# Performance work log

Measured on AMD Instinct MI355X. Metric: run time of the kernel, lower is better.

The kernel has to match this reference:

```python
import jax, jax.numpy as jnp
import numpy as np

H = 64
VOCAB = 128
LN_EPS = 1e-5
NORM_EPS = 1e-12


def _l2norm(k):
    # F.normalize(..., dim=-1): x / max(||x||_2, eps)
    n = jnp.sqrt(jnp.sum(k * k, axis=-1, keepdims=True))
    return k / jnp.maximum(n, NORM_EPS)


def _delta_scan(M0, ks, vs):
    # ks, vs: [L, B, H] time-major; M0: [B, H, H]
    def step(M, kv):
        k, v = kv
        Mk = jnp.einsum('bij,bj->bi', M, k)            # [B,H]
        M = M + (v - Mk)[:, :, None] * k[:, None, :]   # rank-1 update
        return M, None
    M, _ = jax.lax.scan(step, M0, (ks, vs))
    return M


def reference(x, embed, W1, b1, W2, b2, ln_g, ln_b, Wk, Wv, Wq, Wattn, Wout, bout):
    # Encoder: embed -> residual FF -> LayerNorm
    h = embed[x]                                        # [B,L,H]
    ff = jnp.maximum(h @ W1.T + b1, 0.0) @ W2.T + b2
    z = h + ff
    mu = jnp.mean(z, axis=-1, keepdims=True)
    var = jnp.mean((z - mu) ** 2, axis=-1, keepdims=True)
    hidden = (z - mu) / jnp.sqrt(var + LN_EPS) * ln_g + ln_b  # [B,L,H]

    B, L, _ = hidden.shape
    # First delta-rule memory write over all L steps
    ks = _l2norm(hidden @ Wk.T)                         # [B,L,H]
    vs = hidden @ Wv.T                                  # [B,L,H]
    M0 = jnp.zeros((B, H, H), dtype=hidden.dtype)
    M = _delta_scan(M0, jnp.swapaxes(ks, 0, 1), jnp.swapaxes(vs, 0, 1))

    half = L // 2
    slots = jnp.swapaxes(M, 1, 2)                       # [B,H,H] = M^T
    q = hidden[:, :half, :] @ Wattn.T                   # [B,half,H]
    # bmm(q, slots^T) = q @ M
    attn = jax.nn.softmax(jnp.einsum('bth,bhk->btk', q, M) / jnp.sqrt(jnp.asarray(H, hidden.dtype)), axis=-1)
    ctx = jnp.einsum('btk,bkh->bth', attn, slots)       # [B,half,H]

    # Second delta-rule write seeded from M
    ks2 = _l2norm(ctx @ Wk.T)
    vs2 = ctx @ Wv.T
    M2 = _delta_scan(M, jnp.swapaxes(ks2, 0, 1), jnp.swapaxes(vs2, 0, 1))

    q_last = hidden[:, -1, :] @ Wq.T                    # [B,H]
    read = jnp.einsum('bij,bj->bi', M2, q_last)         # [B,H]
    return read @ Wout.T + bout                         # [B,VOCAB]


def setup_inputs() -> dict:
    key = jax.random.key(0)
    ks = jax.random.split(key, 16)
    B, L = 64, 4096
    s = 0.05
    return {
        'x': jax.random.randint(ks[0], (B, L), 0, VOCAB),
        'embed': jax.random.normal(ks[1], (VOCAB, H), jnp.float32) * s,
        'W1': jax.random.normal(ks[2], (2 * H, H), jnp.float32) * s,
        'b1': jnp.zeros((2 * H,), jnp.float32),
        'W2': jax.random.normal(ks[3], (H, 2 * H), jnp.float32) * s,
        'b2': jnp.zeros((H,), jnp.float32),
        'ln_g': jnp.ones((H,), jnp.float32),
        'ln_b': jnp.zeros((H,), jnp.float32),
        'Wk': jax.random.normal(ks[4], (H, H), jnp.float32) * s,
        'Wv': jax.random.normal(ks[5], (H, H), jnp.float32) * s,
        'Wq': jax.random.normal(ks[6], (H, H), jnp.float32) * s,
        'Wattn': jax.random.normal(ks[7], (H, H), jnp.float32) * s,
        'Wout': jax.random.normal(ks[8], (VOCAB, H), jnp.float32) * s,
        'bout': jnp.zeros((VOCAB,), jnp.float32),
    }
```

## Files before the change

### kernel.cpp

```cpp
#include <hip/hip_runtime.h>

#define SEQL 4096
#define NB 64

__device__ __forceinline__ float dpp_xor1_add(float x) {
    int v = __builtin_amdgcn_mov_dpp(__float_as_int(x), 0xB1, 0xF, 0xF, true);
    return x + __int_as_float(v);
}
__device__ __forceinline__ float dpp_xor2_add(float x) {
    int v = __builtin_amdgcn_mov_dpp(__float_as_int(x), 0x4E, 0xF, 0xF, true);
    return x + __int_as_float(v);
}

#define FMA16(A, W, H)                                      \
    A[0]  = fmaf(W.x, H.x, A[0]);  A[1]  = fmaf(W.x, H.y, A[1]);   \
    A[2]  = fmaf(W.x, H.z, A[2]);  A[3]  = fmaf(W.x, H.w, A[3]);   \
    A[4]  = fmaf(W.y, H.x, A[4]);  A[5]  = fmaf(W.y, H.y, A[5]);   \
    A[6]  = fmaf(W.y, H.z, A[6]);  A[7]  = fmaf(W.y, H.w, A[7]);   \
    A[8]  = fmaf(W.z, H.x, A[8]);  A[9]  = fmaf(W.z, H.y, A[9]);   \
    A[10] = fmaf(W.z, H.z, A[10]); A[11] = fmaf(W.z, H.w, A[11]);  \
    A[12] = fmaf(W.w, H.x, A[12]); A[13] = fmaf(W.w, H.y, A[13]);  \
    A[14] = fmaf(W.w, H.z, A[14]); A[15] = fmaf(W.w, H.w, A[15])

__device__ __forceinline__ void proj_tile64(const float* __restrict__ sW,
                                            const float* __restrict__ sA,
                                            int jq, int tq, float* __restrict__ a)
{
#pragma unroll
    for (int u = 0; u < 16; ++u) a[u] = 0.f;
#pragma unroll 4
    for (int i = 0; i < 64; ++i) {
        float4 w  = *reinterpret_cast<const float4*>(&sW[i * 68 + jq]);
        float4 h4 = *reinterpret_cast<const float4*>(&sA[i * 68 + tq]);
        FMA16(a, w, h4);
    }
}

__device__ __forceinline__ void load_w_t(const float* __restrict__ W, int ldw, int col0,
                                         int tid, float4* __restrict__ r)
{
    const int j = tid & 63;
    const int cq0 = tid >> 6;
#pragma unroll
    for (int it = 0; it < 4; ++it)
        r[it] = *reinterpret_cast<const float4*>(&W[(size_t)j * ldw + col0 + (it * 4 + cq0) * 4]);
}
__device__ __forceinline__ void write_w_t(const float4* __restrict__ r,
                                          float* __restrict__ sWb, int tid)
{
    const int j = tid & 63;
    const int cq0 = tid >> 6;
#pragma unroll
    for (int it = 0; it < 4; ++it) {
        const int c = (it * 4 + cq0) * 4;
        sWb[(c + 0) * 68 + j] = r[it].x;
        sWb[(c + 1) * 68 + j] = r[it].y;
        sWb[(c + 2) * 68 + j] = r[it].z;
        sWb[(c + 3) * 68 + j] = r[it].w;
    }
}

__device__ __forceinline__ void stage_w_t(const float* __restrict__ W, int ldw, int col0,
                                          float* __restrict__ sWb, int tid)
{
    float4 r[4];
    load_w_t(W, ldw, col0, tid, r);
    write_w_t(r, sWb, tid);
}
__device__ __forceinline__ void stage_w_n(const float* __restrict__ W,
                                          float* __restrict__ sWb, int tid)
{
#pragma unroll
    for (int it = 0; it < 4; ++it) {
        int item = it * 256 + tid;
        int r = item >> 4, c4 = item & 15;
        float4 w = *reinterpret_cast<const float4*>(&W[(size_t)r * 64 + c4 * 4]);
        *reinterpret_cast<float4*>(&sWb[r * 68 + c4 * 4]) = w;
    }
}

__global__ __launch_bounds__(256) void encoder_kernel(
    const int* __restrict__ x, const float* __restrict__ embed,
    const float* __restrict__ W1, const float* __restrict__ b1,
    const float* __restrict__ W2, const float* __restrict__ b2,
    const float* __restrict__ ln_g, const float* __restrict__ ln_b,
    const float* __restrict__ Wk, const float* __restrict__ Wv,
    const float* __restrict__ Wq,
    float* __restrict__ ks, float* __restrict__ vs,
    float* __restrict__ hidT, float* __restrict__ qlast)
{
    __shared__ __align__(16) float sZ[64 * 68];
    __shared__ __align__(16) float sF[64 * 68];
    __shared__ __align__(16) float sW[64 * 68];

    const int tid = threadIdx.x;
    const size_t g0 = (size_t)blockIdx.x * 64;
    const int b = (int)(g0 >> 12);
    const int l0 = (int)(g0 & (SEQL - 1));
    const int jq = (tid & 15) * 4;
    const int tq = (tid >> 4) * 4;
    const bool doq = (l0 < 2048);
    const bool dolast = (l0 == SEQL - 64);

    float4 pf[4], pf2[4];

    load_w_t(W1, 64, 0, tid, pf);
    for (int idx = tid; idx < 4096; idx += 256) {
        int t = idx >> 6, i = idx & 63;
        sZ[i * 68 + t] = embed[(size_t)x[g0 + t] * 64 + i];
    }
    write_w_t(pf, sW, tid);
    load_w_t(W2, 128, 0, tid, pf2);
    __syncthreads();

    float zacc[16];
#pragma unroll
    for (int u = 0; u < 16; ++u) zacc[u] = 0.f;

    {
        float a[16];
        proj_tile64(sW, sZ, jq, tq, a);
        float4 bb = *reinterpret_cast<const float4*>(&b1[jq]);
        float bv[4] = {bb.x, bb.y, bb.z, bb.w};
#pragma unroll
        for (int u = 0; u < 4; ++u) {
            float4 o;
            o.x = fmaxf(a[u * 4 + 0] + bv[u], 0.f);
            o.y = fmaxf(a[u * 4 + 1] + bv[u], 0.f);
            o.z = fmaxf(a[u * 4 + 2] + bv[u], 0.f);
            o.w = fmaxf(a[u * 4 + 3] + bv[u], 0.f);
            *reinterpret_cast<float4*>(&sF[(jq + u) * 68 + tq]) = o;
        }
    }
    __syncthreads();
    write_w_t(pf2, sW, tid);
    load_w_t(W1 + 4096, 64, 0, tid, pf);
    __syncthreads();
#pragma unroll 4
    for (int p = 0; p < 64; ++p) {
        float4 w  = *reinterpret_cast<const float4*>(&sW[p * 68 + jq]);
        float4 f4 = *reinterpret_cast<const float4*>(&sF[p * 68 + tq]);
        FMA16(zacc, w, f4);
    }
    __syncthreads();
    write_w_t(pf, sW, tid);
    load_w_t(W2, 128, 64, tid, pf2);
    __syncthreads();
    {
        float a[16];
        proj_tile64(sW, sZ, jq, tq, a);
        float4 bb = *reinterpret_cast<const float4*>(&b1[64 + jq]);
        float bv[4] = {bb.x, bb.y, bb.z, bb.w};
#pragma unroll
        for (int u = 0; u < 4; ++u) {
            float4 o;
            o.x = fmaxf(a[u * 4 + 0] + bv[u], 0.f);
            o.y = fmaxf(a[u * 4 + 1] + bv[u], 0.f);
            o.z = fmaxf(a[u * 4 + 2] + bv[u], 0.f);
            o.w = fmaxf(a[u * 4 + 3] + bv[u], 0.f);
            *reinterpret_cast<float4*>(&sF[(jq + u) * 68 + tq]) = o;
        }
    }
    __syncthreads();
    write_w_t(pf2, sW, tid);
    load_w_t(Wk, 64, 0, tid, pf);
    load_w_t(Wv, 64, 0, tid, pf2);
    __syncthreads();
#pragma unroll 4
    for (int p = 0; p < 64; ++p) {
        float4 w  = *reinterpret_cast<const float4*>(&sW[p * 68 + jq]);
        float4 f4 = *reinterpret_cast<const float4*>(&sF[p * 68 + tq]);
        FMA16(zacc, w, f4);
    }

    {
        float z[16];
        float4 b2v = *reinterpret_cast<const float4*>(&b2[jq]);
        float bv[4] = {b2v.x, b2v.y, b2v.z, b2v.w};
#pragma unroll
        for (int u = 0; u < 4; ++u) {
            float4 h4 = *reinterpret_cast<const float4*>(&sZ[(jq + u) * 68 + tq]);
            z[u * 4 + 0] = h4.x + bv[u] + zacc[u * 4 + 0];
            z[u * 4 + 1] = h4.y + bv[u] + zacc[u * 4 + 1];
            z[u * 4 + 2] = h4.z + bv[u] + zacc[u * 4 + 2];
            z[u * 4 + 3] = h4.w + bv[u] + zacc[u * 4 + 3];
        }
        float s[4], ss[4];
#pragma unroll
        for (int v = 0; v < 4; ++v) {
            s[v]  = z[v] + z[4 + v] + z[8 + v] + z[12 + v];
            ss[v] = z[v] * z[v] + z[4 + v] * z[4 + v]
                  + z[8 + v] * z[8 + v] + z[12 + v] * z[12 + v];
        }
#pragma unroll
        for (int m = 1; m <= 8; m <<= 1) {
#pragma unroll
            for (int v = 0; v < 4; ++v) {
                s[v]  += __shfl_xor(s[v], m);
                ss[v] += __shfl_xor(ss[v], m);
            }
        }
        float mu[4], inv[4];
#pragma unroll
        for (int v = 0; v < 4; ++v) {
            mu[v] = s[v] * 0.015625f;
            float var = ss[v] * 0.015625f - mu[v] * mu[v];
            inv[v] = rsqrtf(var + 1e-5f);
        }
        float4 g4  = *reinterpret_cast<const float4*>(&ln_g[jq]);
        float4 be4 = *reinterpret_cast<const float4*>(&ln_b[jq]);
        float gv[4] = {g4.x, g4.y, g4.z, g4.w};
        float bev[4] = {be4.x, be4.y, be4.z, be4.w};
#pragma unroll
        for (int u = 0; u < 4; ++u) {
            float4 o;
            o.x = (z[u * 4 + 0] - mu[0]) * inv[0] * gv[u] + bev[u];
            o.y = (z[u * 4 + 1] - mu[1]) * inv[1] * gv[u] + bev[u];
            o.z = (z[u * 4 + 2] - mu[2]) * inv[2] * gv[u] + bev[u];
            o.w = (z[u * 4 + 3] - mu[3]) * inv[3] * gv[u] + bev[u];
            *reinterpret_cast<float4*>(&sZ[(jq + u) * 68 + tq]) = o;
        }
    }
    __syncthreads();
    write_w_t(pf, sW, tid);
    write_w_t(pf2, sF, tid);
    if (dolast) load_w_t(Wq, 64, 0, tid, pf);
    __syncthreads();

    {
        float a[16];
        proj_tile64(sW, sZ, jq, tq, a);
        float ssq[4];
#pragma unroll
        for (int v = 0; v < 4; ++v)
            ssq[v] = a[v] * a[v] + a[4 + v] * a[4 + v]
                   + a[8 + v] * a[8 + v] + a[12 + v] * a[12 + v];
#pragma unroll
        for (int m = 1; m <= 8; m <<= 1) {
#pragma unroll
            for (int v = 0; v < 4; ++v) ssq[v] += __shfl_xor(ssq[v], m);
        }
#pragma unroll
        for (int v = 0; v < 4; ++v) {
            float sc = 1.f / fmaxf(sqrtf(ssq[v]), 1e-12f);
            float4 o = make_float4(a[v] * sc, a[4 + v] * sc, a[8 + v] * sc, a[12 + v] * sc);
            *reinterpret_cast<float4*>(&ks[(g0 + tq + v) * 64 + jq]) = o;
        }
    }
    {
        float a[16];
        proj_tile64(sF, sZ, jq, tq, a);
#pragma unroll
        for (int v = 0; v < 4; ++v) {
            float4 o = make_float4(a[v], a[4 + v], a[8 + v], a[12 + v]);
            *reinterpret_cast<float4*>(&vs[(g0 + tq + v) * 64 + jq]) = o;
        }
    }

    if (doq) {
#pragma unroll
        for (int it = 0; it < 4; ++it) {
            int item = it * 256 + tid;
            int i = item >> 4, q4 = (item & 15) * 4;
            float4 v = *reinterpret_cast<const float4*>(&sZ[i * 68 + q4]);
            *reinterpret_cast<float4*>(&hidT[((size_t)b * 64 + i) * 2048 + l0 + q4]) = v;
        }
    }

    if (dolast) {
        __syncthreads();
        write_w_t(pf, sW, tid);
        __syncthreads();
        float a[16];
        proj_tile64(sW, sZ, jq, tq, a);
        if ((tid >> 4) == 15) {
            float4 o = make_float4(a[3], a[7], a[11], a[15]);
            *reinterpret_cast<float4*>(&qlast[(size_t)b * 64 + jq]) = o;
        }
    }
}

__global__ __launch_bounds__(256) void precompute_kernel(
    const float* __restrict__ Mbuf, const float* __restrict__ Wattn,
    const float* __restrict__ Wk, const float* __restrict__ Wv,
    float* __restrict__ WAM, float* __restrict__ MK, float* __restrict__ MV)
{
    __shared__ __align__(16) float sM[64 * 68];
    __shared__ __align__(16) float sOp[64 * 68];
    const int b = blockIdx.x;
    const int tid = threadIdx.x;
    const int jq = (tid & 15) * 4;
    const int tq = (tid >> 4) * 4;
    const float* Mb = Mbuf + (size_t)b * 4096;

    stage_w_n(Mb, sM, tid);
    stage_w_n(Wattn, sOp, tid);
    __syncthreads();
    {
        float a[16];
        proj_tile64(sM, sOp, jq, tq, a);
#pragma unroll
        for (int v = 0; v < 4; ++v)
            *reinterpret_cast<float4*>(&WAM[(size_t)b * 4096 + (tq + v) * 64 + jq]) =
                make_float4(a[v], a[4 + v], a[8 + v], a[12 + v]);
    }
    __syncthreads();
    stage_w_t(Wk, 64, 0, sOp, tid);
    __syncthreads();
    {
        float a[16];
        proj_tile64(sM, sOp, jq, tq, a);
#pragma unroll
        for (int v = 0; v < 4; ++v)
            *reinterpret_cast<float4*>(&MK[(size_t)b * 4096 + (tq + v) * 64 + jq]) =
                make_float4(a[v], a[4 + v], a[8 + v], a[12 + v]);
    }
    __syncthreads();
    stage_w_t(Wv, 64, 0, sOp, tid);
    __syncthreads();
    {
        float a[16];
        proj_tile64(sM, sOp, jq, tq, a);
#pragma unroll
        for (int v = 0; v < 4; ++v)
            *reinterpret_cast<float4*>(&MV[(size_t)b * 4096 + (tq + v) * 64 + jq]) =
                make_float4(a[v], a[4 + v], a[8 + v], a[12 + v]);
    }
}

#define STEP2(K0, K1, K2, K3, V)                                                \
    do {                                                                        \
        float dp0 = fmaf(p[0], K0.x, fmaf(p[1], K0.y, fmaf(p[2], K0.z, p[3] * K0.w))); \
        float dp1 = fmaf(p[4], K1.x, fmaf(p[5], K1.y, fmaf(p[6], K1.z, p[7] * K1.w))); \
        float dp2 = fmaf(p[8], K2.x, fmaf(p[9], K2.y, fmaf(p[10], K2.z, p[11] * K2.w))); \
        float dp3 = fmaf(p[12], K3.x, fmaf(p[13], K3.y, fmaf(p[14], K3.z, p[15] * K3.w))); \
        float dq0 = fmaf(q[0], K0.x, fmaf(q[1], K0.y, fmaf(q[2], K0.z, q[3] * K0.w))); \
        float dq1 = fmaf(q[4], K1.x, fmaf(q[5], K1.y, fmaf(q[6], K1.z, q[7] * K1.w))); \
        float dq2 = fmaf(q[8], K2.x, fmaf(q[9], K2.y, fmaf(q[10], K2.z, q[11] * K2.w))); \
        float dq3 = fmaf(q[12], K3.x, fmaf(q[13], K3.y, fmaf(q[14], K3.z, q[15] * K3.w))); \
        float ddp = (dp0 + dp1) + (dp2 + dp3);                                  \
        float ddq = (dq0 + dq1) + (dq2 + dq3);                                  \
        ddp = dpp_xor1_add(ddp);  ddq = dpp_xor1_add(ddq);                      \
        ddp = dpp_xor2_add(ddp);  ddq = dpp_xor2_add(ddq);                      \
        float up = -ddp;                                                        \
        float uq = V - ddq;                                                     \
        p[0] = fmaf(up, K0.x, p[0]);   q[0] = fmaf(uq, K0.x, q[0]);             \
        p[1] = fmaf(up, K0.y, p[1]);   q[1] = fmaf(uq, K0.y, q[1]);             \
        p[2] = fmaf(up, K0.z, p[2]);   q[2] = fmaf(uq, K0.z, q[2]);             \
        p[3] = fmaf(up, K0.w, p[3]);   q[3] = fmaf(uq, K0.w, q[3]);             \
        p[4] = fmaf(up, K1.x, p[4]);   q[4] = fmaf(uq, K1.x, q[4]);             \
        p[5] = fmaf(up, K1.y, p[5]);   q[5] = fmaf(uq, K1.y, q[5]);             \
        p[6] = fmaf(up, K1.z, p[6]);   q[6] = fmaf(uq, K1.z, q[6]);             \
        p[7] = fmaf(up, K1.w, p[7]);   q[7] = fmaf(uq, K1.w, q[7]);             \
        p[8] = fmaf(up, K2.x, p[8]);   q[8] = fmaf(uq, K2.x, q[8]);             \
        p[9] = fmaf(up, K2.y, p[9]);   q[9] = fmaf(uq, K2.y, q[9]);             \
        p[10] = fmaf(up, K2.z, p[10]); q[10] = fmaf(uq, K2.z, q[10]);           \
        p[11] = fmaf(up, K2.w, p[11]); q[11] = fmaf(uq, K2.w, q[11]);           \
        p[12] = fmaf(up, K3.x, p[12]); q[12] = fmaf(uq, K3.x, q[12]);           \
        p[13] = fmaf(up, K3.y, p[13]); q[13] = fmaf(uq, K3.y, q[13]);           \
        p[14] = fmaf(up, K3.z, p[14]); q[14] = fmaf(uq, K3.z, q[14]);           \
        p[15] = fmaf(up, K3.w, p[15]); q[15] = fmaf(uq, K3.w, q[15]);           \
    } while (0)

__global__ __launch_bounds__(256) void chunk_kernel(
    float* __restrict__ ksb, float* __restrict__ vsb, int C)
{
    __shared__ __align__(16) float sk[2][32 * 64];
    __shared__ __align__(16) float sv[2][32 * 64];

    const int job = blockIdx.x;
    const int tid = threadIdx.x;
    const int r = tid >> 2;
    const int c0 = (tid & 3) * 16;
    float* kc = ksb + (size_t)job * C * 64;
    float* vc = vsb + (size_t)job * C * 64;

    float p[16], q[16];
#pragma unroll
    for (int j = 0; j < 16; ++j) { p[j] = (c0 + j == r) ? 1.f : 0.f; q[j] = 0.f; }

    const int nt = C >> 5;
    float4 rk0, rk1, rv0, rv1;

    {
        const float4* gk = reinterpret_cast<const float4*>(kc);
        const float4* gv = reinterpret_cast<const float4*>(vc);
        float4 a0 = gk[tid], a1 = gk[256 + tid];
        float4 b0 = gv[tid], b1 = gv[256 + tid];
        float4* dk = reinterpret_cast<float4*>(sk[0]);
        float4* dv = reinterpret_cast<float4*>(sv[0]);
        dk[tid] = a0; dk[256 + tid] = a1;
        dv[tid] = b0; dv[256 + tid] = b1;
    }
    if (nt > 1) {
        const float4* gk = reinterpret_cast<const float4*>(kc + 2048);
        const float4* gv = reinterpret_cast<const float4*>(vc + 2048);
        rk0 = gk[tid]; rk1 = gk[256 + tid];
        rv0 = gv[tid]; rv1 = gv[256 + tid];
    }
    __syncthreads();

    int cur = 0;
    for (int tile = 0; tile < nt; ++tile) {
        if (tile + 1 < nt) {
            float4* dk = reinterpret_cast<float4*>(sk[cur ^ 1]);
            float4* dv = reinterpret_cast<float4*>(sv[cur ^ 1]);
            dk[tid] = rk0; dk[256 + tid] = rk1;
            dv[tid] = rv0; dv[256 + tid] = rv1;
            if (tile + 2 < nt) {
                const float4* gk = reinterpret_cast<const float4*>(kc + (size_t)(tile + 2) * 2048);
                const float4* gv = reinterpret_cast<const float4*>(vc + (size_t)(tile + 2) * 2048);
                rk0 = gk[tid]; rk1 = gk[256 + tid];
                rv0 = gv[tid]; rv1 = gv[256 + tid];
            }
        }

        const float* kl = sk[cur] + c0;
        const float* vl = sv[cur] + r;
        float4 a0, a1, a2, a3, e0, e1, e2, e3;
        float va, ve;
        {
            const float4* kp = reinterpret_cast<const float4*>(kl);
            a0 = kp[0]; a1 = kp[1]; a2 = kp[2]; a3 = kp[3];
            va = vl[0];
        }
#pragma unroll
        for (int t = 0; t < 32; t += 2) {
            {
                const float4* kp = reinterpret_cast<const float4*>(kl + (t + 1) * 64);
                e0 = kp[0]; e1 = kp[1]; e2 = kp[2]; e3 = kp[3];
                ve = vl[(t + 1) * 64];
            }
            STEP2(a0, a1, a2, a3, va);
            if (t + 2 < 32) {
                const float4* kp = reinterpret_cast<const float4*>(kl + (t + 2) * 64);
                a0 = kp[0]; a1 = kp[1]; a2 = kp[2]; a3 = kp[3];
                va = vl[(t + 2) * 64];
            }
            STEP2(e0, e1, e2, e3, ve);
        }
        __syncthreads();
        cur ^= 1;
    }

    float4* po = reinterpret_cast<float4*>(kc + r * 64 + c0);
    po[0] = make_float4(p[0], p[1], p[2], p[3]);
    po[1] = make_float4(p[4], p[5], p[6], p[7]);
    po[2] = make_float4(p[8], p[9], p[10], p[11]);
    po[3] = make_float4(p[12], p[13], p[14], p[15]);
    float4* qo = reinterpret_cast<float4*>(vc + r * 64 + c0);
    qo[0] = make_float4(q[0], q[1], q[2], q[3]);
    qo[1] = make_float4(q[4], q[5], q[6], q[7]);
    qo[2] = make_float4(q[8], q[9], q[10], q[11]);
    qo[3] = make_float4(q[12], q[13], q[14], q[15]);
}

__global__ __launch_bounds__(256) void combine_kernel(
    const float* __restrict__ Pb, const float* __restrict__ Qb,
    const float* __restrict__ Min, float* __restrict__ Mout,
    int nc, int chunk_stride)
{
    __shared__ __align__(16) float sP[2][64 * 64];
    __shared__ __align__(16) float sM[2][16 * 68];
    const int bb = blockIdx.x;
    const int b = bb >> 2;
    const int r0 = (bb & 3) << 4;
    const int tid = threadIdx.x;
    const int rl = tid >> 4;
    const int j4 = (tid & 15) * 4;
    const int gr = r0 + rl;

    if (Min) {
        *reinterpret_cast<float4*>(&sM[0][rl * 68 + j4]) =
            *reinterpret_cast<const float4*>(Min + ((size_t)b * 64 + gr) * 64 + j4);
    } else {
        *reinterpret_cast<float4*>(&sM[0][rl * 68 + j4]) = make_float4(0.f, 0.f, 0.f, 0.f);
    }
    {
        const float4* g = reinterpret_cast<const float4*>(Pb + (size_t)b * nc * chunk_stride);
        float4* s = reinterpret_cast<float4*>(sP[0]);
        for (int i = tid; i < 1024; i += 256) s[i] = g[i];
    }
    __syncthreads();

    int cur = 0;
    for (int c = 0; c < nc; ++c) {
        const size_t cbase = (size_t)(b * nc + c) * chunk_stride;
        float4 rp0, rp1, rp2, rp3;
        if (c + 1 < nc) {
            const float4* g = reinterpret_cast<const float4*>(Pb + cbase + chunk_stride);
            rp0 = g[tid]; rp1 = g[tid + 256]; rp2 = g[tid + 512]; rp3 = g[tid + 768];
        }
        float4 rq = *reinterpret_cast<const float4*>(Qb + cbase + (size_t)gr * 64 + j4);

        float ax = 0.f, ay = 0.f, az = 0.f, aw = 0.f;
        const float* Mrow = &sM[cur][rl * 68];
        const float* Pl = sP[c & 1];
#pragma unroll 4
        for (int mg = 0; mg < 16; ++mg) {
            float4 a4 = *reinterpret_cast<const float4*>(Mrow + mg * 4);
            float4 p0 = *reinterpret_cast<const float4*>(Pl + (mg * 4 + 0) * 64 + j4);
            float4 p1 = *reinterpret_cast<const float4*>(Pl + (mg * 4 + 1) * 64 + j4);
            float4 p2 = *reinterpret_cast<const float4*>(Pl + (mg * 4 + 2) * 64 + j4);
            float4 p3 = *reinterpret_cast<const float4*>(Pl + (mg * 4 + 3) * 64 + j4);
            ax = fmaf(a4.x, p0.x, ax); ay = fmaf(a4.x, p0.y, ay);
            az = fmaf(a4.x, p0.z, az); aw = fmaf(a4.x, p0.w, aw);
            ax = fmaf(a4.y, p1.x, ax); ay = fmaf(a4.y, p1.y, ay);
            az = fmaf(a4.y, p1.z, az); aw = fmaf(a4.y, p1.w, aw);
            ax = fmaf(a4.z, p2.x, ax); ay = fmaf(a4.z, p2.y, ay);
            az = fmaf(a4.z, p2.z, az); aw = fmaf(a4.z, p2.w, aw);
            ax = fmaf(a4.w, p3.x, ax); ay = fmaf(a4.w, p3.y, ay);
            az = fmaf(a4.w, p3.z, az); aw = fmaf(a4.w, p3.w, aw);
        }
        const int nxt = cur ^ 1;
        *reinterpret_cast<float4*>(&sM[nxt][rl * 68 + j4]) =
            make_float4(ax + rq.x, ay + rq.y, az + rq.z, aw + rq.w);
        if (c + 1 < nc) {
            float4* s = reinterpret_cast<float4*>(sP[(c + 1) & 1]);
            s[tid] = rp0; s[tid + 256] = rp1; s[tid + 512] = rp2; s[tid + 768] = rp3;
        }
        __syncthreads();
        cur = nxt;
    }
    *reinterpret_cast<float4*>(Mout + ((size_t)b * 64 + gr) * 64 + j4) =
        *reinterpret_cast<const float4*>(&sM[cur][rl * 68 + j4]);
}

__global__ __launch_bounds__(256) void attn_kernel(
    const float* __restrict__ hidT, const float* __restrict__ WAM,
    const float* __restrict__ MK, const float* __restrict__ MV,
    float* __restrict__ ks2, float* __restrict__ vs2)
{
    __shared__ __align__(16) float sW1[64 * 68];
    __shared__ __align__(16) float sW2[64 * 68];
    __shared__ __align__(16) float sA[64 * 68];

    const int b = blockIdx.y;
    const int tile0 = blockIdx.x * 64;
    const int tid = threadIdx.x;
    const int jq = (tid & 15) * 4;
    const int tq = (tid >> 4) * 4;
    const size_t qbase = (size_t)b * 2048 + tile0;
    const float* hb = hidT + (size_t)b * 64 * 2048 + tile0;

    float4 pfk[4];
    stage_w_n(WAM + (size_t)b * 4096, sW1, tid);
    stage_w_t(MV + (size_t)b * 4096, 64, 0, sW2, tid);
#pragma unroll
    for (int it = 0; it < 4; ++it) {
        int item = it * 256 + tid;
        int i = item >> 4, q4 = (item & 15) * 4;
        float4 v = *reinterpret_cast<const float4*>(&hb[(size_t)i * 2048 + q4]);
        *reinterpret_cast<float4*>(&sA[i * 68 + q4]) = v;
    }
    load_w_t(MK + (size_t)b * 4096, 64, 0, tid, pfk);
    __syncthreads();

    float a[16];
    proj_tile64(sW1, sA, jq, tq, a);
#pragma unroll
    for (int u = 0; u < 16; ++u) a[u] *= 0.125f;

    {
        float mx[4], sm[4];
#pragma unroll
        for (int v = 0; v < 4; ++v)
            mx[v] = fmaxf(fmaxf(a[v], a[4 + v]), fmaxf(a[8 + v], a[12 + v]));
#pragma unroll
        for (int m = 1; m <= 8; m <<= 1) {
#pragma unroll
            for (int v = 0; v < 4; ++v) mx[v] = fmaxf(mx[v], __shfl_xor(mx[v], m));
        }
#pragma unroll
        for (int v = 0; v < 4; ++v) {
            a[v]      = __expf(a[v]      - mx[v]);
            a[4 + v]  = __expf(a[4 + v]  - mx[v]);
            a[8 + v]  = __expf(a[8 + v]  - mx[v]);
            a[12 + v] = __expf(a[12 + v] - mx[v]);
            sm[v] = a[v] + a[4 + v] + a[8 + v] + a[12 + v];
        }
#pragma unroll
        for (int m = 1; m <= 8; m <<= 1) {
#pragma unroll
            for (int v = 0; v < 4; ++v) sm[v] += __shfl_xor(sm[v], m);
        }
        float rinv[4];
#pragma unroll
        for (int v = 0; v < 4; ++v) rinv[v] = 1.f / sm[v];
#pragma unroll
        for (int v = 0; v < 4; ++v) {
            a[v] *= rinv[v]; a[4 + v] *= rinv[v];
            a[8 + v] *= rinv[v]; a[12 + v] *= rinv[v];
        }
    }
    __syncthreads();
#pragma unroll
    for (int u = 0; u < 4; ++u)
        *reinterpret_cast<float4*>(&sA[(jq + u) * 68 + tq]) =
            make_float4(a[u * 4 + 0], a[u * 4 + 1], a[u * 4 + 2], a[u * 4 + 3]);
    write_w_t(pfk, sW1, tid);
    __syncthreads();

    float ak[16], av[16];
#pragma unroll
    for (int u = 0; u < 16; ++u) { ak[u] = 0.f; av[u] = 0.f; }
#pragma unroll 2
    for (int i = 0; i < 64; ++i) {
        float4 wk = *reinterpret_cast<const float4*>(&sW1[i * 68 + jq]);
        float4 wv = *reinterpret_cast<const float4*>(&sW2[i * 68 + jq]);
        float4 p4 = *reinterpret_cast<const float4*>(&sA[i * 68 + tq]);
        FMA16(ak, wk, p4);
        FMA16(av, wv, p4);
    }

    {
        float ssq[4];
#pragma unroll
        for (int v = 0; v < 4; ++v)
            ssq[v] = ak[v] * ak[v] + ak[4 + v] * ak[4 + v]
                   + ak[8 + v] * ak[8 + v] + ak[12 + v] * ak[12 + v];
#pragma unroll
        for (int m = 1; m <= 8; m <<= 1) {
#pragma unroll
            for (int v = 0; v < 4; ++v) ssq[v] += __shfl_xor(ssq[v], m);
        }
#pragma unroll
        for (int v = 0; v < 4; ++v) {
            float sc = 1.f / fmaxf(sqrtf(ssq[v]), 1e-12f);
            const size_t o = (qbase + tq + v) * 64 + jq;
            *reinterpret_cast<float4*>(&ks2[o]) =
                make_float4(ak[v] * sc, ak[4 + v] * sc, ak[8 + v] * sc, ak[12 + v] * sc);
            *reinterpret_cast<float4*>(&vs2[o]) =
                make_float4(av[v], av[4 + v], av[8 + v], av[12 + v]);
        }
    }
}

__global__ __launch_bounds__(128) void out_kernel(
    const float* __restrict__ M2, const float* __restrict__ qlast,
    const float* __restrict__ Wout, const float* __restrict__ bout,
    float* __restrict__ out)
{
    const int b = blockIdx.x;
    const int tid = threadIdx.x;
    __shared__ float sq[64], sread[64];
    if (tid < 64) sq[tid] = qlast[b * 64 + tid];
    __syncthreads();
    if (tid < 64) {
        const float* Mr = M2 + ((size_t)b * 64 + tid) * 64;
        float acc = 0.f;
        for (int j = 0; j < 64; ++j) acc = fmaf(Mr[j], sq[j], acc);
        sread[tid] = acc;
    }
    __syncthreads();
    float acc = bout[tid];
    for (int h = 0; h < 64; ++h) acc = fmaf(Wout[tid * 64 + h], sread[h], acc);
    out[b * 128 + tid] = acc;
}

extern "C" void kernel_launch(void* const* d_in, const int* in_sizes, int n_in,
                              void* d_out, int out_size, void* d_ws, size_t ws_size,
                              hipStream_t stream)
{
    const int* x        = (const int*)d_in[0];
    const float* embed  = (const float*)d_in[1];
    const float* W1     = (const float*)d_in[2];
    const float* b1     = (const float*)d_in[3];
    const float* W2     = (const float*)d_in[4];
    const float* b2     = (const float*)d_in[5];
    const float* ln_g   = (const float*)d_in[6];
    const float* ln_b   = (const float*)d_in[7];
    const float* Wk     = (const float*)d_in[8];
    const float* Wv     = (const float*)d_in[9];
    const float* Wq     = (const float*)d_in[10];
    const float* Wattn  = (const float*)d_in[11];
    const float* Wout   = (const float*)d_in[12];
    const float* bout   = (const float*)d_in[13];

    float* ws = (float*)d_ws;
    float* ks  = ws;
    float* vs  = ks  + (size_t)NB * SEQL * 64;
    float* hid = vs  + (size_t)NB * SEQL * 64;
    float* ql  = hid + (size_t)NB * 2048 * 64;
    float* M   = ql  + (size_t)NB * 64;
    float* M2  = M   + (size_t)NB * 64 * 64;
    float* WAM = M2  + (size_t)NB * 64 * 64;
    float* MK  = WAM + (size_t)NB * 64 * 64;
    float* MV  = MK  + (size_t)NB * 64 * 64;
    if (ws_size < (size_t)(MV + (size_t)NB * 64 * 64 - ws) * sizeof(float)) return;

    hipLaunchKernelGGL(encoder_kernel, dim3((NB * SEQL) / 64), dim3(256), 0, stream,
                       x, embed, W1, b1, W2, b2, ln_g, ln_b, Wk, Wv, Wq,
                       ks, vs, hid, ql);

    const int C1 = 256, nc1 = SEQL / C1;
    hipLaunchKernelGGL(chunk_kernel, dim3(NB * nc1), dim3(256), 0, stream, ks, vs, C1);
    hipLaunchKernelGGL(combine_kernel, dim3(NB * 4), dim3(256), 0, stream,
                       ks, vs, (const float*)nullptr, M, nc1, C1 * 64);

    hipLaunchKernelGGL(precompute_kernel, dim3(NB), dim3(256), 0, stream,
                       M, Wattn, Wk, Wv, WAM, MK, MV);

    hipLaunchKernelGGL(attn_kernel, dim3(32, NB), dim3(256), 0, stream,
                       hid, WAM, MK, MV, ks, vs);

    const int C2 = 128, nc2 = 2048 / C2;
    hipLaunchKernelGGL(chunk_kernel, dim3(NB * nc2), dim3(256), 0, stream, ks, vs, C2);
    hipLaunchKernelGGL(combine_kernel, dim3(NB * 4), dim3(256), 0, stream,
                       ks, vs, M, M2, nc2, C2 * 64);

    hipLaunchKernelGGL(out_kernel, dim3(NB), dim3(128), 0, stream,
                       M2, ql, Wout, bout, (float*)d_out);
}
```

Baseline: 474.5 us.

## Fold second-scan combine into final readout via backward vector propagation

The second delta-rule pass no longer builds the full final memory matrix M2. The new final kernel starts from q_last and walks the chunk factors (P, Q) in reverse. Each step is a matrix-vector product, so the per-chunk matrix-matrix combine and its kernel launch are dropped. The second-pass chunk size also shrinks, giving more chunks and more parallel chunk work. The cost is a serial loop over more chunks, run by one block per batch, in the final kernel.

```diff
diff --git a/kernel.cpp b/kernel.cpp
--- a/kernel.cpp
+++ b/kernel.cpp
@@ -636,26 +636,87 @@
     }
 }
 
-__global__ __launch_bounds__(128) void out_kernel(
-    const float* __restrict__ M2, const float* __restrict__ qlast,
+__global__ __launch_bounds__(256) void final_kernel(
+    const float* __restrict__ Pb, const float* __restrict__ Qb,
+    const float* __restrict__ Mbuf, const float* __restrict__ qlast,
     const float* __restrict__ Wout, const float* __restrict__ bout,
-    float* __restrict__ out)
-{
+    float* __restrict__ out, int nc, int chunk_stride)
+{
+    __shared__ float s[64], qv[64], rv[64];
     const int b = blockIdx.x;
     const int tid = threadIdx.x;
-    __shared__ float sq[64], sread[64];
-    if (tid < 64) sq[tid] = qlast[b * 64 + tid];
-    __syncthreads();
-    if (tid < 64) {
-        const float* Mr = M2 + ((size_t)b * 64 + tid) * 64;
-        float acc = 0.f;
-        for (int j = 0; j < 64; ++j) acc = fmaf(Mr[j], sq[j], acc);
-        sread[tid] = acc;
-    }
-    __syncthreads();
-    float acc = bout[tid];
-    for (int h = 0; h < 64; ++h) acc = fmaf(Wout[tid * 64 + h], sread[h], acc);
-    out[b * 128 + tid] = acc;
+    const int r = tid >> 2;
+    const int c0 = (tid & 3) * 16;
+
+    if (tid < 64) { s[tid] = qlast[(size_t)b * 64 + tid]; qv[tid] = 0.f; }
+    __syncthreads();
+
+    for (int c = nc - 1; c >= 0; --c) {
+        const size_t base = (size_t)(b * nc + c) * chunk_stride + (size_t)r * 64 + c0;
+        const float4* gp = reinterpret_cast<const float4*>(Pb + base);
+        const float4* gq = reinterpret_cast<const float4*>(Qb + base);
+        float4 P0 = gp[0], P1 = gp[1], P2 = gp[2], P3 = gp[3];
+        float4 Q0 = gq[0], Q1 = gq[1], Q2 = gq[2], Q3 = gq[3];
+        const float4* sv4 = reinterpret_cast<const float4*>(&s[c0]);
+        float4 s0 = sv4[0], s1 = sv4[1], s2 = sv4[2], s3 = sv4[3];
+
+        float dp = 0.f, dq = 0.f;
+        dp = fmaf(P0.x, s0.x, dp); dp = fmaf(P0.y, s0.y, dp);
+        dp = fmaf(P0.z, s0.z, dp); dp = fmaf(P0.w, s0.w, dp);
+        dp = fmaf(P1.x, s1.x, dp); dp = fmaf(P1.y, s1.y, dp);
+        dp = fmaf(P1.z, s1.z, dp); dp = fmaf(P1.w, s1.w, dp);
+        dp = fmaf(P2.x, s2.x, dp); dp = fmaf(P2.y, s2.y, dp);
+        dp = fmaf(P2.z, s2.z, dp); dp = fmaf(P2.w, s2.w, dp);
+        dp = fmaf(P3.x, s3.x, dp); dp = fmaf(P3.y, s3.y, dp);
+        dp = fmaf(P3.z, s3.z, dp); dp = fmaf(P3.w, s3.w, dp);
+        dq = fmaf(Q0.x, s0.x, dq); dq = fmaf(Q0.y, s0.y, dq);
+        dq = fmaf(Q0.z, s0.z, dq); dq = fmaf(Q0.w, s0.w, dq);
+        dq = fmaf(Q1.x, s1.x, dq); dq = fmaf(Q1.y, s1.y, dq);
+        dq = fmaf(Q1.z, s1.z, dq); dq = fmaf(Q1.w, s1.w, dq);
+        dq = fmaf(Q2.x, s2.x, dq); dq = fmaf(Q2.y, s2.y, dq);
+        dq = fmaf(Q2.z, s2.z, dq); dq = fmaf(Q2.w, s2.w, dq);
+        dq = fmaf(Q3.x, s3.x, dq); dq = fmaf(Q3.y, s3.y, dq);
+        dq = fmaf(Q3.z, s3.z, dq); dq = fmaf(Q3.w, s3.w, dq);
+        dp = dpp_xor1_add(dp); dp = dpp_xor2_add(dp);
+        dq = dpp_xor1_add(dq); dq = dpp_xor2_add(dq);
+
+        __syncthreads();
+        if ((tid & 3) == 0) { s[r] = dp; qv[r] += dq; }
+        __syncthreads();
+    }
+
+    {
+        const float4* gm = reinterpret_cast<const float4*>(
+            Mbuf + (size_t)b * 4096 + (size_t)r * 64 + c0);
+        float4 M0 = gm[0], M1 = gm[1], M2v = gm[2], M3 = gm[3];
+        const float4* sv4 = reinterpret_cast<const float4*>(&s[c0]);
+        float4 s0 = sv4[0], s1 = sv4[1], s2 = sv4[2], s3 = sv4[3];
+        float d = 0.f;
+        d = fmaf(M0.x, s0.x, d); d = fmaf(M0.y, s0.y, d);
+        d = fmaf(M0.z, s0.z, d); d = fmaf(M0.w, s0.w, d);
+        d = fmaf(M1.x, s1.x, d); d = fmaf(M1.y, s1.y, d);
+        d = fmaf(M1.z, s1.z, d); d = fmaf(M1.w, s1.w, d);
+        d = fmaf(M2v.x, s2.x, d); d = fmaf(M2v.y, s2.y, d);
+        d = fmaf(M2v.z, s2.z, d); d = fmaf(M2v.w, s2.w, d);
+        d = fmaf(M3.x, s3.x, d); d = fmaf(M3.y, s3.y, d);
+        d = fmaf(M3.z, s3.z, d); d = fmaf(M3.w, s3.w, d);
+        d = dpp_xor1_add(d); d = dpp_xor2_add(d);
+        if ((tid & 3) == 0) rv[r] = d + qv[r];
+    }
+    __syncthreads();
+
+    if (tid < 128) {
+        const float* wr = Wout + (size_t)tid * 64;
+        float a0 = 0.f, a1 = 0.f, a2 = 0.f, a3 = 0.f;
+#pragma unroll
+        for (int h = 0; h < 64; h += 4) {
+            a0 = fmaf(wr[h],     rv[h],     a0);
+            a1 = fmaf(wr[h + 1], rv[h + 1], a1);
+            a2 = fmaf(wr[h + 2], rv[h + 2], a2);
+            a3 = fmaf(wr[h + 3], rv[h + 3], a3);
+        }
+        out[(size_t)b * 128 + tid] = bout[tid] + (a0 + a1) + (a2 + a3);
+    }
 }
 
 extern "C" void kernel_launch(void* const* d_in, const int* in_sizes, int n_in,
@@ -683,8 +744,7 @@
     float* hid = vs  + (size_t)NB * SEQL * 64;
     float* ql  = hid + (size_t)NB * 2048 * 64;
     float* M   = ql  + (size_t)NB * 64;
-    float* M2  = M   + (size_t)NB * 64 * 64;
-    float* WAM = M2  + (size_t)NB * 64 * 64;
+    float* WAM = M   + (size_t)NB * 64 * 64;
     float* MK  = WAM + (size_t)NB * 64 * 64;
     float* MV  = MK  + (size_t)NB * 64 * 64;
     if (ws_size < (size_t)(MV + (size_t)NB * 64 * 64 - ws) * sizeof(float)) return;
@@ -704,11 +764,8 @@
     hipLaunchKernelGGL(attn_kernel, dim3(32, NB), dim3(256), 0, stream,
                        hid, WAM, MK, MV, ks, vs);
 
-    const int C2 = 128, nc2 = 2048 / C2;
+    const int C2 = 64, nc2 = 2048 / C2;
     hipLaunchKernelGGL(chunk_kernel, dim3(NB * nc2), dim3(256), 0, stream, ks, vs, C2);
-    hipLaunchKernelGGL(combine_kernel, dim3(NB * 4), dim3(256), 0, stream,
-                       ks, vs, M, M2, nc2, C2 * 64);
-
-    hipLaunchKernelGGL(out_kernel, dim3(NB), dim3(128), 0, stream,
-                       M2, ql, Wout, bout, (float*)d_out);
-}
+    hipLaunchKernelGGL(final_kernel, dim3(NB), dim3(256), 0, stream,
+                       ks, vs, M, ql, Wout, bout, (float*)d_out, nc2, C2 * 64);
+}
```

After: 479.2 us. Within noise of the previous version (+1.0%).
